# Kernel tuning notes

Hardware: AMD Instinct MI355X
Metric: run time of the kernel (lower is better)

The kernel has to match this reference:

```python
import jax, jax.numpy as jnp
import numpy as np
import math

D_MODEL = 1024
NHEAD = 16
D_K = D_MODEL // NHEAD
NUM_LAYERS = 4
D_FF = 4096
SEQ = 2048
BATCH = 1
EPS = 1e-5


def _layer_norm(x, g, b):
    mu = jnp.mean(x, axis=-1, keepdims=True)
    var = jnp.mean((x - mu) ** 2, axis=-1, keepdims=True)
    return (x - mu) * jax.lax.rsqrt(var + EPS) * g + b


def setup_inputs() -> dict:
    key = jax.random.key(0)
    ks = jax.random.split(key, 16)
    s = 0.02
    L, D, F = NUM_LAYERS, D_MODEL, D_FF
    inp = {
        "x": jax.random.normal(ks[0], (BATCH, SEQ, D), dtype=jnp.float32),
        "wq": jax.random.normal(ks[1], (L, D, D), dtype=jnp.float32) * s,
        "bq": jnp.zeros((L, D), dtype=jnp.float32),
        "wk": jax.random.normal(ks[2], (L, D, D), dtype=jnp.float32) * s,
        "bk": jnp.zeros((L, D), dtype=jnp.float32),
        "wv": jax.random.normal(ks[3], (L, D, D), dtype=jnp.float32) * s,
        "bv": jnp.zeros((L, D), dtype=jnp.float32),
        "wo": jax.random.normal(ks[4], (L, D, D), dtype=jnp.float32) * s,
        "bo": jnp.zeros((L, D), dtype=jnp.float32),
        "w1": jax.random.normal(ks[5], (L, D, F), dtype=jnp.float32) * s,
        "b1": jnp.zeros((L, F), dtype=jnp.float32),
        "w2": jax.random.normal(ks[6], (L, F, D), dtype=jnp.float32) * s,
        "b2": jnp.zeros((L, D), dtype=jnp.float32),
        "ln1_g": jnp.ones((L, D), dtype=jnp.float32),
        "ln1_b": jnp.zeros((L, D), dtype=jnp.float32),
        "ln2_g": jnp.ones((L, D), dtype=jnp.float32),
        "ln2_b": jnp.zeros((L, D), dtype=jnp.float32),
    }
    return inp


def _transformer(x, wq, bq, wk, bk, wv, bv, wo, bo, w1, b1, w2, b2,
                 ln1_g, ln1_b, ln2_g, ln2_b):
    B, S, D = x.shape
    scale = math.sqrt(D_K)
    for l in range(NUM_LAYERS):
        # multi-head self-attention (manual QKV matmul + softmax + matmul)
        q = (x @ wq[l] + bq[l]).reshape(B, S, NHEAD, D_K).transpose(0, 2, 1, 3)
        k = (x @ wk[l] + bk[l]).reshape(B, S, NHEAD, D_K).transpose(0, 2, 1, 3)
        v = (x @ wv[l] + bv[l]).reshape(B, S, NHEAD, D_K).transpose(0, 2, 1, 3)
        scores = jnp.einsum('bhqd,bhkd->bhqk', q, k) / scale  # [B,H,S,S]
        attn = jax.nn.softmax(scores, axis=-1)
        ctx = jnp.einsum('bhqk,bhkd->bhqd', attn, v)
        ctx = ctx.transpose(0, 2, 1, 3).reshape(B, S, D)
        attn_out = ctx @ wo[l] + bo[l]
        x = _layer_norm(x + attn_out, ln1_g[l], ln1_b[l])
        # feed-forward network with gelu
        h = jax.nn.gelu(x @ w1[l] + b1[l])
        ffn_out = h @ w2[l] + b2[l]
        x = _layer_norm(x + ffn_out, ln2_g[l], ln2_b[l])
    return x


def reference(x, wq, bq, wk, bk, wv, bv, wo, bo, w1, b1, w2, b2,
              ln1_g, ln1_b, ln2_g, ln2_b):
    return _transformer(x, wq, bq, wk, bk, wv, bv, wo, bo, w1, b1, w2, b2,
                        ln1_g, ln1_b, ln2_g, ln2_b)
```

## Files before the change

kernel.cpp:

```cpp
#include <hip/hip_runtime.h>
#include <hip/hip_bf16.h>
#include <math.h>

typedef __hip_bfloat16 bf16;
typedef __attribute__((ext_vector_type(8))) short bf16x8;
typedef __attribute__((ext_vector_type(4))) short bf16x4;
typedef __attribute__((ext_vector_type(4))) float f32x4;

#define EPI_NONE 0
#define EPI_BIAS_BF16 1
#define EPI_BIAS_GELU_BF16 2

#define CLOG 0.18033688f

__device__ __forceinline__ void gload16(const void* g, void* l) {
  __builtin_amdgcn_global_load_lds((const __attribute__((address_space(1))) void*)g,
                                   (__attribute__((address_space(3))) void*)l, 16, 0, 0);
}

__device__ __forceinline__ float gelu_tanh(float x) {
  const float c = 0.7978845608028654f;
  float t = tanhf(c * (x + 0.044715f * x * x * x));
  return 0.5f * x * (1.0f + t);
}

__device__ __forceinline__ short bf16bits(float x) {
  bf16 h = __float2bfloat16(x);
  return *reinterpret_cast<const short*>(&h);
}

template<int BM, int BN, int BK, int EPI, typename CT>
__global__ __launch_bounds__(256) void gemm_bt(
    const bf16* __restrict__ A, long sAz, int lda,
    const bf16* __restrict__ Bt, long sBz, int ldb,
    CT* __restrict__ C, long sCz, int ldc,
    const float* __restrict__ bias,
    int K, float scale)
{
  constexpr int WM = BM / 2, WN = BN / 2;
  constexpr int MI = WM / 16, NJ = WN / 16;
  constexpr int NA = (BM * BK * 2) / 4096;
  constexpr int NB = (BN * BK * 2) / 4096;
  constexpr int ROWB = BK * 2;
  __shared__ __align__(16) bf16 As[BM * BK];
  __shared__ __align__(16) bf16 Bs[BN * BK];
  const int t = threadIdx.x;
  const int lane = t & 63, w = t >> 6;
  const int wm = (w >> 1) * WM, wn = (w & 1) * WN;
  const int quad = lane >> 4, r16 = lane & 15;
  const long z = blockIdx.z;
  const bf16* Ab = A + z * sAz + (long)blockIdx.y * BM * lda;
  const bf16* Bb = Bt + z * sBz + (long)blockIdx.x * BN * ldb;

  f32x4 acc[MI][NJ];
  #pragma unroll
  for (int i = 0; i < MI; ++i)
    #pragma unroll
    for (int j = 0; j < NJ; ++j)
      acc[i][j] = (f32x4){0.f, 0.f, 0.f, 0.f};

  for (int k0 = 0; k0 < K; k0 += BK) {
    __syncthreads();
    #pragma unroll
    for (int s = 0; s < NA; ++s) {
      int Lb = s * 4096 + t * 16;
      int row = Lb / ROWB, colb = Lb % ROWB;
      gload16((const char*)Ab + (long)row * (lda * 2) + k0 * 2 + colb, (char*)As + Lb);
    }
    #pragma unroll
    for (int s = 0; s < NB; ++s) {
      int Lb = s * 4096 + t * 16;
      int row = Lb / ROWB, colb = Lb % ROWB;
      gload16((const char*)Bb + (long)row * (ldb * 2) + k0 * 2 + colb, (char*)Bs + Lb);
    }
    __syncthreads();

    #pragma unroll
    for (int kk = 0; kk < BK / 32; ++kk) {
      bf16x8 af[MI], bfv[NJ];
      #pragma unroll
      for (int i = 0; i < MI; ++i)
        af[i] = *(const bf16x8*)&As[(wm + i * 16 + r16) * BK + kk * 32 + quad * 8];
      #pragma unroll
      for (int j = 0; j < NJ; ++j)
        bfv[j] = *(const bf16x8*)&Bs[(wn + j * 16 + r16) * BK + kk * 32 + quad * 8];
      #pragma unroll
      for (int i = 0; i < MI; ++i)
        #pragma unroll
        for (int j = 0; j < NJ; ++j)
          acc[i][j] = __builtin_amdgcn_mfma_f32_16x16x32_bf16(af[i], bfv[j], acc[i][j], 0, 0, 0);
    }
  }

  CT* Cb = C + z * sCz;
  #pragma unroll
  for (int i = 0; i < MI; ++i) {
    #pragma unroll
    for (int j = 0; j < NJ; ++j) {
      int col = blockIdx.x * BN + wn + j * 16 + r16;
      float bvv = 0.f;
      if constexpr (EPI == EPI_BIAS_BF16 || EPI == EPI_BIAS_GELU_BF16)
        bvv = bias[col];
      #pragma unroll
      for (int r = 0; r < 4; ++r) {
        long row = (long)blockIdx.y * BM + wm + i * 16 + quad * 4 + r;
        float val = acc[i][j][r] * scale + bvv;
        if constexpr (EPI == EPI_BIAS_GELU_BF16) val = gelu_tanh(val);
        if constexpr (sizeof(CT) == 2)
          Cb[row * (long)ldc + col] = __float2bfloat16(val);
        else
          Cb[row * (long)ldc + col] = val;
      }
    }
  }
}

__global__ __launch_bounds__(256) void flash_attn(
    const bf16* __restrict__ qkv, const bf16* __restrict__ vT,
    float* __restrict__ Osp, float2* __restrict__ ml, int kts)
{
  constexpr int SEQ = 2048, LDP = 72, LDPP = 80;
  __shared__ __align__(16) bf16 Ks[64 * LDP];
  __shared__ __align__(16) bf16 VTs[64 * LDP];
  __shared__ __align__(16) bf16 Ps[64 * LDPP];

  const int t = threadIdx.x;
  const int lane = t & 63, w = t >> 6;
  const int quad = lane >> 4, r16 = lane & 15;
  const int wq0 = w * 16;
  const int s0 = blockIdx.x * 64;
  const int h = blockIdx.y;
  const int split = blockIdx.z;
  const int kt0 = split * kts, ktN = kt0 + kts;

  bf16x8 af_q[2];
  {
    const bf16* qp = qkv + (long)(s0 + wq0 + r16) * 3072 + h * 64 + quad * 8;
    af_q[0] = *(const bf16x8*)(qp);
    af_q[1] = *(const bf16x8*)(qp + 32);
  }

  const bf16* kp[2]; const bf16* vp[2];
  int krow[2], kcolb[2];
  #pragma unroll
  for (int s = 0; s < 2; ++s) {
    int Lb = s * 4096 + t * 16;
    krow[s] = Lb >> 7; kcolb[s] = Lb & 127;
    kp[s] = qkv + 1024 + (long)h * 64 + (long)krow[s] * 3072 + (kcolb[s] >> 1);
    vp[s] = vT + (long)(h * 64 + krow[s]) * SEQ + (kcolb[s] >> 1);
  }

  int4 rk[2], rv[2];
  #pragma unroll
  for (int s = 0; s < 2; ++s) {
    rk[s] = *(const int4*)(kp[s] + (long)kt0 * 64 * 3072);
    rv[s] = *(const int4*)(vp[s] + (long)kt0 * 64);
  }

  f32x4 O[4];
  float m_s = -1e30f, l_s = 0.f;
  #pragma unroll
  for (int jd = 0; jd < 4; ++jd) O[jd] = (f32x4){0.f, 0.f, 0.f, 0.f};

  for (int kt = kt0; kt < ktN; ++kt) {
    __syncthreads();
    #pragma unroll
    for (int s = 0; s < 2; ++s) {
      *(int4*)((char*)Ks + (krow[s] * LDP * 2) + kcolb[s]) = rk[s];
      *(int4*)((char*)VTs + (krow[s] * LDP * 2) + kcolb[s]) = rv[s];
    }
    __syncthreads();

    if (kt + 1 < ktN) {
      long k0n = (long)(kt + 1) * 64;
      #pragma unroll
      for (int s = 0; s < 2; ++s) {
        rk[s] = *(const int4*)(kp[s] + k0n * 3072);
        rv[s] = *(const int4*)(vp[s] + k0n);
      }
    }

    f32x4 sc[4];
    #pragma unroll
    for (int j = 0; j < 4; ++j) sc[j] = (f32x4){0.f, 0.f, 0.f, 0.f};
    #pragma unroll
    for (int kk = 0; kk < 2; ++kk) {
      bf16x8 bk_f[4];
      #pragma unroll
      for (int j = 0; j < 4; ++j)
        bk_f[j] = *(const bf16x8*)&Ks[(j * 16 + r16) * LDP + kk * 32 + quad * 8];
      #pragma unroll
      for (int j = 0; j < 4; ++j)
        sc[j] = __builtin_amdgcn_mfma_f32_16x16x32_bf16(bk_f[j], af_q[kk], sc[j], 0, 0, 0);
    }

    float mj[4];
    #pragma unroll
    for (int j = 0; j < 4; ++j)
      mj[j] = fmaxf(fmaxf(sc[j][0], sc[j][1]), fmaxf(sc[j][2], sc[j][3]));
    float mx = fmaxf(fmaxf(mj[0], mj[1]), fmaxf(mj[2], mj[3]));
    mx = fmaxf(mx, __shfl_xor(mx, 16));
    mx = fmaxf(mx, __shfl_xor(mx, 32));
    float m_new = fmaxf(m_s, mx * CLOG);
    float alpha = exp2f(m_s - m_new);
    m_s = m_new;
    float p[4][4], sj[4];
    #pragma unroll
    for (int j = 0; j < 4; ++j) {
      #pragma unroll
      for (int r = 0; r < 4; ++r)
        p[j][r] = exp2f(fmaf(sc[j][r], CLOG, -m_new));
      sj[j] = (p[j][0] + p[j][1]) + (p[j][2] + p[j][3]);
    }
    float rs = (sj[0] + sj[1]) + (sj[2] + sj[3]);
    rs += __shfl_xor(rs, 16);
    rs += __shfl_xor(rs, 32);
    l_s = l_s * alpha + rs;

    float ar[4];
    #pragma unroll
    for (int r = 0; r < 4; ++r)
      ar[r] = __shfl(alpha, quad * 20 + r);
    #pragma unroll
    for (int jd = 0; jd < 4; ++jd)
      #pragma unroll
      for (int r = 0; r < 4; ++r)
        O[jd][r] *= ar[r];

    {
      bf16* pr = &Ps[(wq0 + r16) * LDPP + quad * 4];
      #pragma unroll
      for (int j = 0; j < 4; ++j) {
        bf16x4 pk;
        #pragma unroll
        for (int r = 0; r < 4; ++r)
          pk[r] = bf16bits(p[j][r]);
        *(bf16x4*)(pr + j * 16) = pk;
      }
    }

    #pragma unroll
    for (int kk = 0; kk < 2; ++kk) {
      bf16x8 af_p, bv_f[4];
      af_p = *(const bf16x8*)&Ps[(wq0 + r16) * LDPP + kk * 32 + quad * 8];
      #pragma unroll
      for (int jd = 0; jd < 4; ++jd)
        bv_f[jd] = *(const bf16x8*)&VTs[(jd * 16 + r16) * LDP + kk * 32 + quad * 8];
      #pragma unroll
      for (int jd = 0; jd < 4; ++jd)
        O[jd] = __builtin_amdgcn_mfma_f32_16x16x32_bf16(af_p, bv_f[jd], O[jd], 0, 0, 0);
    }
  }

  float* Ob = Osp + (long)split * SEQ * 1024;
  #pragma unroll
  for (int r = 0; r < 4; ++r) {
    long row = s0 + wq0 + quad * 4 + r;
    #pragma unroll
    for (int jd = 0; jd < 4; ++jd)
      Ob[row * 1024 + h * 64 + jd * 16 + r16] = O[jd][r];
  }
  if (quad == 0)
    ml[((long)(split * 16 + h)) * SEQ + (s0 + wq0 + r16)] = make_float2(m_s, l_s);
}

__global__ __launch_bounds__(256) void attn_combine(
    const float* __restrict__ Osp, const float2* __restrict__ ml,
    bf16* __restrict__ ctx, int nsplit)
{
  constexpr long SD = 2048L * 1024L;
  const int s = blockIdx.x;
  const int t = threadIdx.x;
  #pragma unroll
  for (int i = 0; i < 4; ++i) {
    int c = t + i * 256;
    int h = c >> 6;
    float mC = -1e30f;
    for (int sp = 0; sp < nsplit; ++sp)
      mC = fmaxf(mC, ml[(long)(sp * 16 + h) * 2048 + s].x);
    float denom = 0.f, num = 0.f;
    for (int sp = 0; sp < nsplit; ++sp) {
      float2 a = ml[(long)(sp * 16 + h) * 2048 + s];
      float wv = exp2f(a.x - mC);
      denom += a.y * wv;
      num += Osp[sp * SD + (long)s * 1024 + c] * wv;
    }
    ctx[(long)s * 1024 + c] = __float2bfloat16(num / denom);
  }
}

__global__ __launch_bounds__(256) void transpose_cast(
    const float* __restrict__ in, bf16* __restrict__ out, int R, int C)
{
  __shared__ bf16 tile[32][33];
  const int tx = threadIdx.x, ty = threadIdx.y;
  const int r0 = blockIdx.y * 32, c0 = blockIdx.x * 32;
  #pragma unroll
  for (int d = 0; d < 32; d += 8)
    tile[ty + d][tx] = __float2bfloat16(in[(long)(r0 + ty + d) * C + c0 + tx]);
  __syncthreads();
  #pragma unroll
  for (int d = 0; d < 32; d += 8)
    out[(long)(c0 + ty + d) * R + r0 + tx] = tile[tx][ty + d];
}

__global__ __launch_bounds__(256) void transpose_cast3(
    const float* __restrict__ w0, const float* __restrict__ w1p,
    const float* __restrict__ w2p, bf16* __restrict__ out, int R, int C)
{
  __shared__ bf16 tile[32][33];
  const float* in = (blockIdx.z == 0) ? w0 : (blockIdx.z == 1) ? w1p : w2p;
  bf16* o = out + (long)blockIdx.z * R * C;
  const int tx = threadIdx.x, ty = threadIdx.y;
  const int r0 = blockIdx.y * 32, c0 = blockIdx.x * 32;
  #pragma unroll
  for (int d = 0; d < 32; d += 8)
    tile[ty + d][tx] = __float2bfloat16(in[(long)(r0 + ty + d) * C + c0 + tx]);
  __syncthreads();
  #pragma unroll
  for (int d = 0; d < 32; d += 8)
    o[(long)(c0 + ty + d) * R + r0 + tx] = tile[tx][ty + d];
}

__global__ __launch_bounds__(256) void transpose_bf16(
    const bf16* __restrict__ in, bf16* __restrict__ out, int R, int C, int ldin)
{
  __shared__ bf16 tile[32][33];
  const int tx = threadIdx.x, ty = threadIdx.y;
  const int r0 = blockIdx.y * 32, c0 = blockIdx.x * 32;
  #pragma unroll
  for (int d = 0; d < 32; d += 8)
    tile[ty + d][tx] = in[(long)(r0 + ty + d) * ldin + c0 + tx];
  __syncthreads();
  #pragma unroll
  for (int d = 0; d < 32; d += 8)
    out[(long)(c0 + ty + d) * R + r0 + tx] = tile[tx][ty + d];
}

__device__ __forceinline__ float blk_sum(float v, float* sh) {
  #pragma unroll
  for (int o = 32; o > 0; o >>= 1) v += __shfl_down(v, o);
  __syncthreads();
  if ((threadIdx.x & 63) == 0) sh[threadIdx.x >> 6] = v;
  __syncthreads();
  return sh[0] + sh[1] + sh[2] + sh[3];
}

__global__ __launch_bounds__(256) void ln_residual2(
    float* __restrict__ X, const float* __restrict__ d0, const float* __restrict__ d1,
    const float* __restrict__ bias,
    const float* __restrict__ g, const float* __restrict__ b,
    bf16* __restrict__ xb)
{
  __shared__ float sh[4];
  const int t = threadIdx.x;
  const long base = (long)blockIdx.x * 1024;
  float v[4]; float s = 0.f;
  #pragma unroll
  for (int i = 0; i < 4; ++i) {
    int c = t + i * 256;
    float val = X[base + c] + d0[base + c] + d1[base + c] + bias[c];
    v[i] = val; s += val;
  }
  s = blk_sum(s, sh);
  const float mu = s * (1.f / 1024.f);
  float s2 = 0.f;
  #pragma unroll
  for (int i = 0; i < 4; ++i) { float d = v[i] - mu; s2 += d * d; }
  s2 = blk_sum(s2, sh);
  const float rs = rsqrtf(s2 * (1.f / 1024.f) + 1e-5f);
  #pragma unroll
  for (int i = 0; i < 4; ++i) {
    int c = t + i * 256;
    float o = (v[i] - mu) * rs * g[c] + b[c];
    X[base + c] = o;
    xb[base + c] = __float2bfloat16(o);
  }
}

__global__ __launch_bounds__(256) void init_x(
    const float* __restrict__ xin, float* __restrict__ X, bf16* __restrict__ xb, int n)
{
  for (int i = blockIdx.x * 256 + threadIdx.x; i < n; i += gridDim.x * 256) {
    float v = xin[i];
    X[i] = v;
    xb[i] = __float2bfloat16(v);
  }
}

__global__ __launch_bounds__(256) void copy_out(
    const float* __restrict__ X, float* __restrict__ out, int n)
{
  for (int i = blockIdx.x * 256 + threadIdx.x; i < n; i += gridDim.x * 256)
    out[i] = X[i];
}

__global__ __launch_bounds__(256) void concat_bias(
    const float* __restrict__ bq, const float* __restrict__ bk,
    const float* __restrict__ bv, float* __restrict__ out, int n)
{
  for (int i = blockIdx.x * 256 + threadIdx.x; i < n; i += gridDim.x * 256) {
    int l = i / 3072, r = i % 3072;
    int j = r / 1024, c = r % 1024;
    const float* src = (j == 0) ? bq : (j == 1) ? bk : bv;
    out[i] = src[l * 1024 + c];
  }
}

extern "C" void kernel_launch(void* const* d_in, const int* in_sizes, int n_in,
                              void* d_out, int out_size, void* d_ws, size_t ws_size,
                              hipStream_t stream) {
  constexpr int S = 2048, D = 1024, F = 4096, L = 4;
  const float* xin = (const float*)d_in[0];
  const float* wq = (const float*)d_in[1];
  const float* bq = (const float*)d_in[2];
  const float* wk = (const float*)d_in[3];
  const float* bk = (const float*)d_in[4];
  const float* wv = (const float*)d_in[5];
  const float* bvp = (const float*)d_in[6];
  const float* wo = (const float*)d_in[7];
  const float* bo = (const float*)d_in[8];
  const float* w1 = (const float*)d_in[9];
  const float* b1 = (const float*)d_in[10];
  const float* w2 = (const float*)d_in[11];
  const float* b2 = (const float*)d_in[12];
  const float* ln1g = (const float*)d_in[13];
  const float* ln1b = (const float*)d_in[14];
  const float* ln2g = (const float*)d_in[15];
  const float* ln2b = (const float*)d_in[16];

  const int nsplit = (ws_size >= 78u * 1024 * 1024) ? 4 : 2;
  const int kts = 32 / nsplit;

  char* p = (char*)d_ws;
  float* X    = (float*)p; p += (long)S * D * 4;
  float* tmpf = (float*)p; p += (long)nsplit * S * D * 4;
  bf16* xb    = (bf16*)p;  p += (long)S * D * 2;
  bf16* qkv   = (bf16*)p;
  bf16* hb    = (bf16*)p;  p += (long)S * 3 * D * 2;
  bf16* ctx   = (bf16*)p;  p += (long)S * D * 2;
  bf16* vT    = (bf16*)p;  p += (long)S * D * 2;
  bf16* wT    = (bf16*)p;  p += (long)F * D * 2;
  float* bias3= (float*)p; p += (long)L * 3 * D * 4;
  float2* ml  = (float2*)p; p += (long)nsplit * 16 * S * 8;

  init_x<<<2048, 256, 0, stream>>>(xin, X, xb, S * D);
  concat_bias<<<48, 256, 0, stream>>>(bq, bk, bvp, bias3, L * 3 * D);

  for (int l = 0; l < L; ++l) {
    transpose_cast3<<<dim3(D / 32, D / 32, 3), dim3(32, 8), 0, stream>>>(
        wq + (long)l * D * D, wk + (long)l * D * D, wv + (long)l * D * D, wT, D, D);
    gemm_bt<128, 64, 64, EPI_BIAS_BF16, bf16><<<dim3(3 * D / 64, S / 128, 1), 256, 0, stream>>>(
        xb, 0L, D, wT, 0L, D, qkv, 0L, 3 * D, bias3 + l * 3 * D, D, 1.f);

    transpose_bf16<<<dim3(D / 32, S / 32), dim3(32, 8), 0, stream>>>(qkv + 2 * D, vT, S, D, 3 * D);

    flash_attn<<<dim3(S / 64, 16, nsplit), 256, 0, stream>>>(qkv, vT, tmpf, ml, kts);
    attn_combine<<<S, 256, 0, stream>>>(tmpf, ml, ctx, nsplit);

    transpose_cast<<<dim3(D / 32, D / 32), dim3(32, 8), 0, stream>>>(wo + (long)l * D * D, wT, D, D);
    gemm_bt<128, 64, 64, EPI_NONE, float><<<dim3(D / 64, S / 128, 2), 256, 0, stream>>>(
        ctx, (long)(D / 2), D, wT, (long)(D / 2), D, tmpf, (long)S * D, D, nullptr, D / 2, 1.f);
    ln_residual2<<<S, 256, 0, stream>>>(X, tmpf, tmpf + (long)S * D, bo + l * D,
                                        ln1g + l * D, ln1b + l * D, xb);

    transpose_cast<<<dim3(F / 32, D / 32), dim3(32, 8), 0, stream>>>(w1 + (long)l * D * F, wT, D, F);
    gemm_bt<128, 128, 64, EPI_BIAS_GELU_BF16, bf16><<<dim3(F / 128, S / 128, 1), 256, 0, stream>>>(
        xb, 0L, D, wT, 0L, D, hb, 0L, F, b1 + l * F, D, 1.f);
    transpose_cast<<<dim3(D / 32, F / 32), dim3(32, 8), 0, stream>>>(w2 + (long)l * F * D, wT, F, D);
    gemm_bt<128, 64, 64, EPI_NONE, float><<<dim3(D / 64, S / 128, 2), 256, 0, stream>>>(
        hb, (long)(F / 2), F, wT, (long)(F / 2), F, tmpf, (long)S * D, D, nullptr, F / 2, 1.f);
    ln_residual2<<<S, 256, 0, stream>>>(X, tmpf, tmpf + (long)S * D, b2 + l * D,
                                        ln2g + l * D, ln2b + l * D, xb);
  }
  copy_out<<<2048, 256, 0, stream>>>(X, (float*)d_out, S * D);
}
```

Baseline: 1.175 ms.

## Widen flash-attention blocks to 128 queries, fix split count, shrink FFN1 tile

The flash-attention kernel now runs 512 threads (8 waves) per block and covers 128 query rows, so each K/V tile staged in shared memory serves twice as many queries. Each thread now loads one K/V vector instead of two, and the P buffer is doubled. The KV split count is fixed at 2 instead of depending on workspace size. The FFN1 GEMM switches from 128x128 to 128x64 tiles, which doubles its block count. This trades grid parallelism and per-block register budget for better K/V reuse and more FFN1 blocks.

```diff
diff --git a/kernel.cpp b/kernel.cpp
--- a/kernel.cpp
+++ b/kernel.cpp
@@ -115,20 +115,20 @@
   }
 }
 
-__global__ __launch_bounds__(256) void flash_attn(
+__global__ __launch_bounds__(512) void flash_attn(
     const bf16* __restrict__ qkv, const bf16* __restrict__ vT,
     float* __restrict__ Osp, float2* __restrict__ ml, int kts)
 {
   constexpr int SEQ = 2048, LDP = 72, LDPP = 80;
   __shared__ __align__(16) bf16 Ks[64 * LDP];
   __shared__ __align__(16) bf16 VTs[64 * LDP];
-  __shared__ __align__(16) bf16 Ps[64 * LDPP];
+  __shared__ __align__(16) bf16 Ps[128 * LDPP];
 
   const int t = threadIdx.x;
   const int lane = t & 63, w = t >> 6;
   const int quad = lane >> 4, r16 = lane & 15;
   const int wq0 = w * 16;
-  const int s0 = blockIdx.x * 64;
+  const int s0 = blockIdx.x * 128;
   const int h = blockIdx.y;
   const int split = blockIdx.z;
   const int kt0 = split * kts, ktN = kt0 + kts;
@@ -140,22 +140,13 @@
     af_q[1] = *(const bf16x8*)(qp + 32);
   }
 
-  const bf16* kp[2]; const bf16* vp[2];
-  int krow[2], kcolb[2];
-  #pragma unroll
-  for (int s = 0; s < 2; ++s) {
-    int Lb = s * 4096 + t * 16;
-    krow[s] = Lb >> 7; kcolb[s] = Lb & 127;
-    kp[s] = qkv + 1024 + (long)h * 64 + (long)krow[s] * 3072 + (kcolb[s] >> 1);
-    vp[s] = vT + (long)(h * 64 + krow[s]) * SEQ + (kcolb[s] >> 1);
-  }
-
-  int4 rk[2], rv[2];
-  #pragma unroll
-  for (int s = 0; s < 2; ++s) {
-    rk[s] = *(const int4*)(kp[s] + (long)kt0 * 64 * 3072);
-    rv[s] = *(const int4*)(vp[s] + (long)kt0 * 64);
-  }
+  const int Lb = t * 16;
+  const int krow = Lb >> 7, kcolb = Lb & 127;
+  const bf16* kp = qkv + 1024 + (long)h * 64 + (long)krow * 3072 + (kcolb >> 1);
+  const bf16* vp = vT + (long)(h * 64 + krow) * SEQ + (kcolb >> 1);
+
+  int4 rk = *(const int4*)(kp + (long)kt0 * 64 * 3072);
+  int4 rv = *(const int4*)(vp + (long)kt0 * 64);
 
   f32x4 O[4];
   float m_s = -1e30f, l_s = 0.f;
@@ -164,20 +155,14 @@
 
   for (int kt = kt0; kt < ktN; ++kt) {
     __syncthreads();
-    #pragma unroll
-    for (int s = 0; s < 2; ++s) {
-      *(int4*)((char*)Ks + (krow[s] * LDP * 2) + kcolb[s]) = rk[s];
-      *(int4*)((char*)VTs + (krow[s] * LDP * 2) + kcolb[s]) = rv[s];
-    }
+    *(int4*)((char*)Ks + (krow * LDP * 2) + kcolb) = rk;
+    *(int4*)((char*)VTs + (krow * LDP * 2) + kcolb) = rv;
     __syncthreads();
 
     if (kt + 1 < ktN) {
       long k0n = (long)(kt + 1) * 64;
-      #pragma unroll
-      for (int s = 0; s < 2; ++s) {
-        rk[s] = *(const int4*)(kp[s] + k0n * 3072);
-        rv[s] = *(const int4*)(vp[s] + k0n);
-      }
+      rk = *(const int4*)(kp + k0n * 3072);
+      rv = *(const int4*)(vp + k0n);
     }
 
     f32x4 sc[4];
@@ -429,7 +414,7 @@
   const float* ln2g = (const float*)d_in[15];
   const float* ln2b = (const float*)d_in[16];
 
-  const int nsplit = (ws_size >= 78u * 1024 * 1024) ? 4 : 2;
+  const int nsplit = 2;
   const int kts = 32 / nsplit;
 
   char* p = (char*)d_ws;
@@ -455,7 +440,7 @@
 
     transpose_bf16<<<dim3(D / 32, S / 32), dim3(32, 8), 0, stream>>>(qkv + 2 * D, vT, S, D, 3 * D);
 
-    flash_attn<<<dim3(S / 64, 16, nsplit), 256, 0, stream>>>(qkv, vT, tmpf, ml, kts);
+    flash_attn<<<dim3(S / 128, 16, nsplit), 512, 0, stream>>>(qkv, vT, tmpf, ml, kts);
     attn_combine<<<S, 256, 0, stream>>>(tmpf, ml, ctx, nsplit);
 
     transpose_cast<<<dim3(D / 32, D / 32), dim3(32, 8), 0, stream>>>(wo + (long)l * D * D, wT, D, D);
@@ -465,7 +450,7 @@
                                         ln1g + l * D, ln1b + l * D, xb);
 
     transpose_cast<<<dim3(F / 32, D / 32), dim3(32, 8), 0, stream>>>(w1 + (long)l * D * F, wT, D, F);
-    gemm_bt<128, 128, 64, EPI_BIAS_GELU_BF16, bf16><<<dim3(F / 128, S / 128, 1), 256, 0, stream>>>(
+    gemm_bt<128, 64, 64, EPI_BIAS_GELU_BF16, bf16><<<dim3(F / 64, S / 128, 1), 256, 0, stream>>>(
         xb, 0L, D, wT, 0L, D, hb, 0L, F, b1 + l * F, D, 1.f);
     transpose_cast<<<dim3(D / 32, F / 32), dim3(32, 8), 0, stream>>>(w2 + (long)l * F * D, wT, F, D);
     gemm_bt<128, 64, 64, EPI_NONE, float><<<dim3(D / 64, S / 128, 2), 256, 0, stream>>>(
```

New measurement: 1.002 ms. 14.7% less time.
